# Kernel tuning notes

Measured on AMD Instinct MI355X. Metric: run time of the kernel, lower is better.

The kernel has to match this reference:

```python
import jax, jax.numpy as jnp
import numpy as np

NOISE_EPS = 0.01
TOP_K = 2


def setup_inputs() -> dict:
    key = jax.random.key(0)
    k1, k2, k3, k4 = jax.random.split(key, 4)
    B, S, D, E = 4, 4096, 2048, 64
    x = jax.random.normal(k1, (B, S, D), dtype=jnp.float32)
    raw_noise = jax.random.normal(k2, (B, S, E), dtype=jnp.float32)
    # gating_mlp: single Linear(D -> E), init std=0.02, zero bias
    W_gate = 0.02 * jax.random.normal(k3, (E, D), dtype=jnp.float32)
    b_gate = jnp.zeros((E,), dtype=jnp.float32)
    # noise_projection: Linear(D -> E, bias=False), init std=1/sqrt(D)
    W_noise = (1.0 / np.sqrt(D)) * jax.random.normal(k4, (E, D), dtype=jnp.float32)
    return {"x": x, "raw_noise": raw_noise, "W_gate": W_gate, "b_gate": b_gate, "W_noise": W_noise}


def reference(x, raw_noise, W_gate, b_gate, W_noise):
    # gate logits: [B,S,E]
    logits = jnp.einsum("bsd,ed->bse", x, W_gate) + b_gate
    # noisy top-k routing (training path)
    noise_stddev = jax.nn.softplus(jnp.einsum("bsd,ed->bse", x, W_noise)) + NOISE_EPS
    noisy = logits + raw_noise * noise_stddev
    top_v, top_i = jax.lax.top_k(noisy, TOP_K)            # [B,S,K]
    top_p = jax.nn.softmax(top_v.astype(jnp.float32), axis=-1).astype(noisy.dtype)
    B, S, E = noisy.shape
    T = B * S
    flat_logits = noisy.reshape(T, E)
    flat_i = top_i.reshape(T, TOP_K)
    flat_p = top_p.reshape(T, TOP_K)
    sparse = jnp.zeros((T, E), dtype=noisy.dtype).at[jnp.arange(T)[:, None], flat_i].set(flat_p)
    # aux load-balancing loss
    indicator = (sparse > 0.0).astype(jnp.float32)
    fraction_routed = indicator.sum(axis=0) / T           # f_e
    router_probs = jax.nn.softmax(flat_logits.astype(jnp.float32), axis=-1)
    avg_prob = router_probs.mean(axis=0)                  # p_e
    aux_loss = jnp.sum(fraction_routed * avg_prob) * E
    return sparse.reshape(B, S, E), aux_loss.astype(noisy.dtype)
```

## Files before the change

### kernel.cpp

```cpp
#include <hip/hip_runtime.h>
#include <math.h>

#define TOK 16384
#define DD  2048
#define EE  64
#define MT  32
#define KCW 32

typedef _Float16 half8  __attribute__((ext_vector_type(8)));
typedef float    floatx4 __attribute__((ext_vector_type(4)));

__global__ void build_wf(const float* __restrict__ Wg, const float* __restrict__ Wn,
                         _Float16* __restrict__ wf) {
  int tid  = blockIdx.x * 256 + threadIdx.x;
  int lane = tid & 63;
  int kc   = (tid >> 6) & 63;
  int ct   = tid >> 12;
  int col  = (ct & 3) * 16 + (lane & 15);
  int k    = kc * 32 + (lane >> 4) * 8;
  const float* W = (ct < 4) ? Wg : Wn;
  const float* src = W + (size_t)col * DD + k;
  float4 a = *reinterpret_cast<const float4*>(src);
  float4 b = *reinterpret_cast<const float4*>(src + 4);
  float v[8] = {a.x, a.y, a.z, a.w, b.x, b.y, b.z, b.w};
  half8 hi, lo;
#pragma unroll
  for (int j = 0; j < 8; ++j) {
    _Float16 h = (_Float16)v[j];
    hi[j] = h;
    lo[j] = (_Float16)(v[j] - (float)h);
  }
  size_t base = (((size_t)(kc * 8 + ct) * 2 + 0) * 64 + lane) * 8;
  *reinterpret_cast<half8*>(wf + base)       = hi;
  *reinterpret_cast<half8*>(wf + base + 512) = lo;
}

#define KBODY(kc, CUR, NXT)                                                        \
  {                                                                                \
    half8 Ah[2], Al[2];                                                            \
    _Pragma("unroll")                                                              \
    for (int mt = 0; mt < 2; ++mt) {                                               \
      float v[8] = {Aa[CUR][mt].x, Aa[CUR][mt].y, Aa[CUR][mt].z, Aa[CUR][mt].w,    \
                    Ab[CUR][mt].x, Ab[CUR][mt].y, Ab[CUR][mt].z, Ab[CUR][mt].w};   \
      _Pragma("unroll")                                                            \
      for (int j = 0; j < 8; ++j) {                                                \
        _Float16 h = (_Float16)v[j];                                               \
        Ah[mt][j] = h;                                                             \
        Al[mt][j] = (_Float16)(v[j] - (float)h);                                   \
      }                                                                            \
    }                                                                              \
    if ((kc) + 2 < KCW) {                                                          \
      _Pragma("unroll")                                                            \
      for (int mt = 0; mt < 2; ++mt) {                                             \
        Aa[CUR][mt] = *reinterpret_cast<const float4*>(xp[mt] + ((kc) + 2) * 32);  \
        Ab[CUR][mt] = *reinterpret_cast<const float4*>(xp[mt] + ((kc) + 2) * 32 + 4); \
      }                                                                            \
    }                                                                              \
    if ((kc) + 1 < KCW) {                                                          \
      _Pragma("unroll")                                                            \
      for (int f = 0; f < 16; ++f) Bf[NXT][f] = wp[((kc) + 1) * 1024 + f * 64];    \
    }                                                                              \
    _Pragma("unroll")                                                              \
    for (int mt = 0; mt < 2; ++mt)                                                 \
      _Pragma("unroll")                                                            \
      for (int ct = 0; ct < 8; ++ct)                                               \
        acc[mt][ct] = __builtin_amdgcn_mfma_f32_16x16x32_f16(                      \
            Ah[mt], Bf[CUR][ct * 2 + 0], acc[mt][ct], 0, 0, 0);                    \
    _Pragma("unroll")                                                              \
    for (int mt = 0; mt < 2; ++mt)                                                 \
      _Pragma("unroll")                                                            \
      for (int ct = 0; ct < 8; ++ct)                                               \
        acc[mt][ct] = __builtin_amdgcn_mfma_f32_16x16x32_f16(                      \
            Ah[mt], Bf[CUR][ct * 2 + 1], acc[mt][ct], 0, 0, 0);                    \
    _Pragma("unroll")                                                              \
    for (int mt = 0; mt < 2; ++mt)                                                 \
      _Pragma("unroll")                                                            \
      for (int ct = 0; ct < 8; ++ct)                                               \
        acc[mt][ct] = __builtin_amdgcn_mfma_f32_16x16x32_f16(                      \
            Al[mt], Bf[CUR][ct * 2 + 0], acc[mt][ct], 0, 0, 0);                    \
  }

__global__ __launch_bounds__(128, 1)
void gating_kernel(const float* __restrict__ x, const float* __restrict__ rn,
                   const _Float16* __restrict__ wf, const float* __restrict__ bg,
                   float* __restrict__ out,
                   float* __restrict__ cnt_g, float* __restrict__ psum_g) {
  __shared__ float Pacc[64 * 64];
  __shared__ float Vb[MT * 65];
  __shared__ float Eb[MT * 65];
  __shared__ float isum[MT];
  __shared__ int   ti[MT * 2];
  __shared__ float tp[MT * 2];

  const int t  = threadIdx.x;
  const int w  = t >> 6;
  const int l  = t & 63;
  const int q  = l >> 4;
  const int cl = l & 15;
  const int t0 = blockIdx.x * MT;

  const float* xp[2];
  xp[0] = x + (size_t)(t0 + cl) * DD + w * (KCW * 32) + q * 8;
  xp[1] = xp[0] + (size_t)16 * DD;

  const half8* wp = reinterpret_cast<const half8*>(wf) + (size_t)(w * KCW) * 16 * 64 + l;

  floatx4 acc[2][8];
#pragma unroll
  for (int mt = 0; mt < 2; ++mt)
#pragma unroll
    for (int ct = 0; ct < 8; ++ct) acc[mt][ct] = (floatx4)0.f;

  float4 Aa[2][2], Ab[2][2];
  half8  Bf[2][16];

#pragma unroll
  for (int mt = 0; mt < 2; ++mt) {
    Aa[0][mt] = *reinterpret_cast<const float4*>(xp[mt]);
    Ab[0][mt] = *reinterpret_cast<const float4*>(xp[mt] + 4);
    Aa[1][mt] = *reinterpret_cast<const float4*>(xp[mt] + 32);
    Ab[1][mt] = *reinterpret_cast<const float4*>(xp[mt] + 36);
  }
#pragma unroll
  for (int f = 0; f < 16; ++f) Bf[0][f] = wp[f * 64];

  for (int kc2 = 0; kc2 < KCW; kc2 += 2) {
    KBODY(kc2, 0, 1)
    KBODY(kc2 + 1, 1, 0)
  }

  if (w == 1) {
#pragma unroll
    for (int mt = 0; mt < 2; ++mt)
#pragma unroll
      for (int ct = 0; ct < 8; ++ct)
#pragma unroll
        for (int r = 0; r < 4; ++r)
          Pacc[((mt * 8 + ct) * 4 + r) * 64 + l] = acc[mt][ct][r];
  }
  __syncthreads();

  if (w == 0) {
#pragma unroll
    for (int mt = 0; mt < 2; ++mt)
#pragma unroll
      for (int ct = 0; ct < 8; ++ct)
#pragma unroll
        for (int r = 0; r < 4; ++r)
          acc[mt][ct][r] += Pacc[((mt * 8 + ct) * 4 + r) * 64 + l];

    float bgv[4];
#pragma unroll
    for (int ct = 0; ct < 4; ++ct) bgv[ct] = bg[ct * 16 + cl];

#pragma unroll
    for (int mt = 0; mt < 2; ++mt)
#pragma unroll
      for (int ct = 0; ct < 4; ++ct)
#pragma unroll
        for (int r = 0; r < 4; ++r) {
          const int tk = mt * 16 + q * 4 + r;
          const int c  = ct * 16 + cl;
          float gt = acc[mt][ct][r] + bgv[ct];
          float h  = acc[mt][ct + 4][r];
          float sp = (h > 20.f) ? h : log1pf(expf(h));
          float v  = gt + rn[(size_t)(t0 + tk) * EE + c] * (sp + 0.01f);
          Vb[tk * 65 + c] = v;
          Eb[tk * 65 + c] = expf(v);
        }
  }
  __syncthreads();

  if (t < MT) {
    float v1 = -1e30f, v2 = -1e30f;
    int   i1 = 0, i2 = 0;
    float s = 0.f;
    for (int e = 0; e < EE; ++e) {
      float v = Vb[t * 65 + e];
      s += Eb[t * 65 + e];
      if (v > v1)      { v2 = v1; i2 = i1; v1 = v; i1 = e; }
      else if (v > v2) { v2 = v;  i2 = e; }
    }
    isum[t] = 1.f / s;
    ti[t * 2 + 0] = i1; ti[t * 2 + 1] = i2;
    float e2 = expf(v2 - v1);
    float dn = 1.f + e2;
    tp[t * 2 + 0] = 1.f / dn;
    tp[t * 2 + 1] = e2 / dn;
  }
  __syncthreads();

#pragma unroll
  for (int i = 0; i < 4; ++i) {
    const int idx = t + i * 128;
    const int m   = idx >> 4;
    const int c0  = (idx & 15) * 4;
    const int i1 = ti[m * 2 + 0], i2 = ti[m * 2 + 1];
    const float p1 = tp[m * 2 + 0], p2 = tp[m * 2 + 1];
    float o[4];
#pragma unroll
    for (int j = 0; j < 4; ++j) {
      const int col = c0 + j;
      o[j] = (col == i1) ? p1 : ((col == i2) ? p2 : 0.f);
    }
    *reinterpret_cast<float4*>(out + (size_t)(t0 + m) * EE + c0) =
        make_float4(o[0], o[1], o[2], o[3]);
  }

  if (t < EE) {
    float s = 0.f;
    int   cn = 0;
#pragma unroll
    for (int m = 0; m < MT; ++m) {
      s  += Eb[m * 65 + t] * isum[m];
      cn += (ti[m * 2 + 0] == t) + (ti[m * 2 + 1] == t);
    }
    atomicAdd(&psum_g[t], s);
    atomicAdd(&cnt_g[t], (float)cn);
  }
}

__global__ void aux_kernel(const float* __restrict__ cnt_g,
                           const float* __restrict__ psum_g,
                           float* __restrict__ out) {
  int e = threadIdx.x;
  float v = cnt_g[e] * psum_g[e];
#pragma unroll
  for (int o = 32; o > 0; o >>= 1) v += __shfl_down(v, o);
  if (e == 0)
    out[(size_t)TOK * EE] = v * ((float)EE / ((float)TOK * (float)TOK));
}

extern "C" void kernel_launch(void* const* d_in, const int* in_sizes, int n_in,
                              void* d_out, int out_size, void* d_ws, size_t ws_size,
                              hipStream_t stream) {
  const float* x  = (const float*)d_in[0];
  const float* rn = (const float*)d_in[1];
  const float* Wg = (const float*)d_in[2];
  const float* bg = (const float*)d_in[3];
  const float* Wn = (const float*)d_in[4];
  float* out    = (float*)d_out;
  float* cnt_g  = (float*)d_ws;
  float* psum_g = cnt_g + EE;
  _Float16* wf  = (_Float16*)((float*)d_ws + 128);

  hipMemsetAsync(d_ws, 0, 2 * EE * sizeof(float), stream);
  build_wf<<<128, 256, 0, stream>>>(Wg, Wn, wf);
  gating_kernel<<<TOK / MT, 128, 0, stream>>>(x, rn, wf, bg, out, cnt_g, psum_g);
  aux_kernel<<<1, 64, 0, stream>>>(cnt_g, psum_g, out);
}
```

Baseline: 259.8 us.

## Split gating GEMM across 8 waves by column group and K half

```diff
diff --git a/kernel.cpp b/kernel.cpp
--- a/kernel.cpp
+++ b/kernel.cpp
@@ -30,144 +30,160 @@
     hi[j] = h;
     lo[j] = (_Float16)(v[j] - (float)h);
   }
-  size_t base = (((size_t)(kc * 8 + ct) * 2 + 0) * 64 + lane) * 8;
+  int cw4 = ct & 3;
+  int nf  = ct >> 2;
+  size_t base = (((size_t)(kc * 16 + cw4 * 4 + nf * 2) ) * 64 + lane) * 8;
   *reinterpret_cast<half8*>(wf + base)       = hi;
   *reinterpret_cast<half8*>(wf + base + 512) = lo;
 }
 
-#define KBODY(kc, CUR, NXT)                                                        \
-  {                                                                                \
-    half8 Ah[2], Al[2];                                                            \
-    _Pragma("unroll")                                                              \
-    for (int mt = 0; mt < 2; ++mt) {                                               \
-      float v[8] = {Aa[CUR][mt].x, Aa[CUR][mt].y, Aa[CUR][mt].z, Aa[CUR][mt].w,    \
-                    Ab[CUR][mt].x, Ab[CUR][mt].y, Ab[CUR][mt].z, Ab[CUR][mt].w};   \
-      _Pragma("unroll")                                                            \
-      for (int j = 0; j < 8; ++j) {                                                \
-        _Float16 h = (_Float16)v[j];                                               \
-        Ah[mt][j] = h;                                                             \
-        Al[mt][j] = (_Float16)(v[j] - (float)h);                                   \
-      }                                                                            \
-    }                                                                              \
-    if ((kc) + 2 < KCW) {                                                          \
-      _Pragma("unroll")                                                            \
-      for (int mt = 0; mt < 2; ++mt) {                                             \
-        Aa[CUR][mt] = *reinterpret_cast<const float4*>(xp[mt] + ((kc) + 2) * 32);  \
-        Ab[CUR][mt] = *reinterpret_cast<const float4*>(xp[mt] + ((kc) + 2) * 32 + 4); \
-      }                                                                            \
-    }                                                                              \
-    if ((kc) + 1 < KCW) {                                                          \
-      _Pragma("unroll")                                                            \
-      for (int f = 0; f < 16; ++f) Bf[NXT][f] = wp[((kc) + 1) * 1024 + f * 64];    \
-    }                                                                              \
-    _Pragma("unroll")                                                              \
-    for (int mt = 0; mt < 2; ++mt)                                                 \
-      _Pragma("unroll")                                                            \
-      for (int ct = 0; ct < 8; ++ct)                                               \
-        acc[mt][ct] = __builtin_amdgcn_mfma_f32_16x16x32_f16(                      \
-            Ah[mt], Bf[CUR][ct * 2 + 0], acc[mt][ct], 0, 0, 0);                    \
-    _Pragma("unroll")                                                              \
-    for (int mt = 0; mt < 2; ++mt)                                                 \
-      _Pragma("unroll")                                                            \
-      for (int ct = 0; ct < 8; ++ct)                                               \
-        acc[mt][ct] = __builtin_amdgcn_mfma_f32_16x16x32_f16(                      \
-            Ah[mt], Bf[CUR][ct * 2 + 1], acc[mt][ct], 0, 0, 0);                    \
-    _Pragma("unroll")                                                              \
-    for (int mt = 0; mt < 2; ++mt)                                                 \
-      _Pragma("unroll")                                                            \
-      for (int ct = 0; ct < 8; ++ct)                                               \
-        acc[mt][ct] = __builtin_amdgcn_mfma_f32_16x16x32_f16(                      \
-            Al[mt], Bf[CUR][ct * 2 + 0], acc[mt][ct], 0, 0, 0);                    \
-  }
-
-__global__ __launch_bounds__(128, 1)
+#define KBODY(CUR, NXT, AOFFE, BOFFH8, DOA, DOB)                                   \
+  {                                                                               \
+    half8 Ah[2], Al[2];                                                           \
+    _Pragma("unroll")                                                             \
+    for (int mt = 0; mt < 2; ++mt) {                                              \
+      float v[8] = {Aa[CUR][mt].x, Aa[CUR][mt].y, Aa[CUR][mt].z, Aa[CUR][mt].w,   \
+                    Ab[CUR][mt].x, Ab[CUR][mt].y, Ab[CUR][mt].z, Ab[CUR][mt].w};  \
+      _Pragma("unroll")                                                           \
+      for (int j = 0; j < 8; ++j) {                                               \
+        _Float16 h = (_Float16)v[j];                                              \
+        Ah[mt][j] = h;                                                            \
+        Al[mt][j] = (_Float16)(v[j] - (float)h);                                  \
+      }                                                                           \
+    }                                                                             \
+    if (DOA) {                                                                    \
+      Aa[CUR][0] = *reinterpret_cast<const float4*>(xq0 + (AOFFE));               \
+      Ab[CUR][0] = *reinterpret_cast<const float4*>(xq0 + (AOFFE) + 4);           \
+      Aa[CUR][1] = *reinterpret_cast<const float4*>(xq1 + (AOFFE));               \
+      Ab[CUR][1] = *reinterpret_cast<const float4*>(xq1 + (AOFFE) + 4);           \
+    }                                                                             \
+    if (DOB) {                                                                    \
+      _Pragma("unroll")                                                           \
+      for (int f = 0; f < 4; ++f) Bf[NXT][f] = wq[(BOFFH8) + f * 64];             \
+    }                                                                             \
+    _Pragma("unroll")                                                             \
+    for (int mt = 0; mt < 2; ++mt)                                                \
+      _Pragma("unroll")                                                           \
+      for (int nf = 0; nf < 2; ++nf)                                              \
+        acc[mt][nf] = __builtin_amdgcn_mfma_f32_16x16x32_f16(                     \
+            Ah[mt], Bf[CUR][nf * 2 + 0], acc[mt][nf], 0, 0, 0);                   \
+    _Pragma("unroll")                                                             \
+    for (int mt = 0; mt < 2; ++mt)                                                \
+      _Pragma("unroll")                                                           \
+      for (int nf = 0; nf < 2; ++nf)                                              \
+        acc[mt][nf] = __builtin_amdgcn_mfma_f32_16x16x32_f16(                     \
+            Ah[mt], Bf[CUR][nf * 2 + 1], acc[mt][nf], 0, 0, 0);                   \
+    _Pragma("unroll")                                                             \
+    for (int mt = 0; mt < 2; ++mt)                                                \
+      _Pragma("unroll")                                                           \
+      for (int nf = 0; nf < 2; ++nf)                                              \
+        acc[mt][nf] = __builtin_amdgcn_mfma_f32_16x16x32_f16(                     \
+            Al[mt], Bf[CUR][nf * 2 + 0], acc[mt][nf], 0, 0, 0);                   \
+  }
+
+__global__ __launch_bounds__(512, 4)
 void gating_kernel(const float* __restrict__ x, const float* __restrict__ rn,
                    const _Float16* __restrict__ wf, const float* __restrict__ bg,
                    float* __restrict__ out,
                    float* __restrict__ cnt_g, float* __restrict__ psum_g) {
-  __shared__ float Pacc[64 * 64];
+  __shared__ float Pacc[4096];
   __shared__ float Vb[MT * 65];
   __shared__ float Eb[MT * 65];
   __shared__ float isum[MT];
   __shared__ int   ti[MT * 2];
   __shared__ float tp[MT * 2];
 
-  const int t  = threadIdx.x;
-  const int w  = t >> 6;
-  const int l  = t & 63;
-  const int q  = l >> 4;
-  const int cl = l & 15;
-  const int t0 = blockIdx.x * MT;
-
-  const float* xp[2];
-  xp[0] = x + (size_t)(t0 + cl) * DD + w * (KCW * 32) + q * 8;
-  xp[1] = xp[0] + (size_t)16 * DD;
-
-  const half8* wp = reinterpret_cast<const half8*>(wf) + (size_t)(w * KCW) * 16 * 64 + l;
-
-  floatx4 acc[2][8];
+  const int t   = threadIdx.x;
+  const int w   = t >> 6;
+  const int cw4 = w & 3;
+  const int kw  = w >> 2;
+  const int l   = t & 63;
+  const int q   = l >> 4;
+  const int cl  = l & 15;
+  const int t0  = blockIdx.x * MT;
+
+  const float* xb0 = x + (size_t)(t0 + cl) * DD + kw * (KCW * 32) + q * 8;
+  const float* xb1 = xb0 + (size_t)16 * DD;
+
+  const half8* wb = reinterpret_cast<const half8*>(wf)
+                  + (size_t)kw * (KCW * 1024) + cw4 * 256 + l;
+
+  floatx4 acc[2][2];
 #pragma unroll
   for (int mt = 0; mt < 2; ++mt)
 #pragma unroll
-    for (int ct = 0; ct < 8; ++ct) acc[mt][ct] = (floatx4)0.f;
+    for (int nf = 0; nf < 2; ++nf) acc[mt][nf] = (floatx4)0.f;
 
   float4 Aa[2][2], Ab[2][2];
-  half8  Bf[2][16];
+  half8  Bf[2][4];
 
 #pragma unroll
   for (int mt = 0; mt < 2; ++mt) {
-    Aa[0][mt] = *reinterpret_cast<const float4*>(xp[mt]);
-    Ab[0][mt] = *reinterpret_cast<const float4*>(xp[mt] + 4);
-    Aa[1][mt] = *reinterpret_cast<const float4*>(xp[mt] + 32);
-    Ab[1][mt] = *reinterpret_cast<const float4*>(xp[mt] + 36);
-  }
-#pragma unroll
-  for (int f = 0; f < 16; ++f) Bf[0][f] = wp[f * 64];
-
-  for (int kc2 = 0; kc2 < KCW; kc2 += 2) {
-    KBODY(kc2, 0, 1)
-    KBODY(kc2 + 1, 1, 0)
-  }
-
-  if (w == 1) {
-#pragma unroll
-    for (int mt = 0; mt < 2; ++mt)
-#pragma unroll
-      for (int ct = 0; ct < 8; ++ct)
+    const float* xb = (mt == 0) ? xb0 : xb1;
+    Aa[0][mt] = *reinterpret_cast<const float4*>(xb);
+    Ab[0][mt] = *reinterpret_cast<const float4*>(xb + 4);
+    Aa[1][mt] = *reinterpret_cast<const float4*>(xb + 32);
+    Ab[1][mt] = *reinterpret_cast<const float4*>(xb + 36);
+  }
+#pragma unroll
+  for (int f = 0; f < 4; ++f) Bf[0][f] = wb[f * 64];
+
+  const float* xq0 = xb0 + 64;
+  const float* xq1 = xb1 + 64;
+  const half8* wq  = wb + 1024;
+
+  for (int it = 0; it < (KCW - 2) / 2; ++it) {
+    KBODY(0, 1, 0, 0, 1, 1)
+    KBODY(1, 0, 32, 1024, 1, 1)
+    xq0 += 64; xq1 += 64; wq += 2048;
+  }
+  KBODY(0, 1, 0, 0, 0, 1)
+  KBODY(1, 0, 0, 0, 0, 0)
+
+  float bgv = 0.f;
+  float rnv[2][4];
+  if (kw == 0) {
+    bgv = bg[cw4 * 16 + cl];
+#pragma unroll
+    for (int mt = 0; mt < 2; ++mt)
+#pragma unroll
+      for (int r = 0; r < 4; ++r)
+        rnv[mt][r] = rn[(size_t)(t0 + mt * 16 + q * 4 + r) * EE + cw4 * 16 + cl];
+  }
+
+  if (kw == 1) {
+#pragma unroll
+    for (int mt = 0; mt < 2; ++mt)
+#pragma unroll
+      for (int nf = 0; nf < 2; ++nf)
 #pragma unroll
         for (int r = 0; r < 4; ++r)
-          Pacc[((mt * 8 + ct) * 4 + r) * 64 + l] = acc[mt][ct][r];
+          Pacc[(cw4 * 16 + (mt * 2 + nf) * 4 + r) * 64 + l] = acc[mt][nf][r];
   }
   __syncthreads();
 
-  if (w == 0) {
-#pragma unroll
-    for (int mt = 0; mt < 2; ++mt)
-#pragma unroll
-      for (int ct = 0; ct < 8; ++ct)
+  if (kw == 0) {
+#pragma unroll
+    for (int mt = 0; mt < 2; ++mt)
+#pragma unroll
+      for (int nf = 0; nf < 2; ++nf)
 #pragma unroll
         for (int r = 0; r < 4; ++r)
-          acc[mt][ct][r] += Pacc[((mt * 8 + ct) * 4 + r) * 64 + l];
-
-    float bgv[4];
-#pragma unroll
-    for (int ct = 0; ct < 4; ++ct) bgv[ct] = bg[ct * 16 + cl];
-
-#pragma unroll
-    for (int mt = 0; mt < 2; ++mt)
-#pragma unroll
-      for (int ct = 0; ct < 4; ++ct)
-#pragma unroll
-        for (int r = 0; r < 4; ++r) {
-          const int tk = mt * 16 + q * 4 + r;
-          const int c  = ct * 16 + cl;
-          float gt = acc[mt][ct][r] + bgv[ct];
-          float h  = acc[mt][ct + 4][r];
-          float sp = (h > 20.f) ? h : log1pf(expf(h));
-          float v  = gt + rn[(size_t)(t0 + tk) * EE + c] * (sp + 0.01f);
-          Vb[tk * 65 + c] = v;
-          Eb[tk * 65 + c] = expf(v);
-        }
+          acc[mt][nf][r] += Pacc[(cw4 * 16 + (mt * 2 + nf) * 4 + r) * 64 + l];
+
+#pragma unroll
+    for (int mt = 0; mt < 2; ++mt)
+#pragma unroll
+      for (int r = 0; r < 4; ++r) {
+        const int tk = mt * 16 + q * 4 + r;
+        const int c  = cw4 * 16 + cl;
+        float gt = acc[mt][0][r] + bgv;
+        float h  = acc[mt][1][r];
+        float sp = (h > 20.f) ? h : log1pf(expf(h));
+        float v  = gt + rnv[mt][r] * (sp + 0.01f);
+        Vb[tk * 65 + c] = v;
+        Eb[tk * 65 + c] = expf(v);
+      }
   }
   __syncthreads();
 
@@ -190,11 +206,9 @@
   }
   __syncthreads();
 
-#pragma unroll
-  for (int i = 0; i < 4; ++i) {
-    const int idx = t + i * 128;
-    const int m   = idx >> 4;
-    const int c0  = (idx & 15) * 4;
+  {
+    const int m  = t >> 4;
+    const int c0 = (t & 15) * 4;
     const int i1 = ti[m * 2 + 0], i2 = ti[m * 2 + 1];
     const float p1 = tp[m * 2 + 0], p2 = tp[m * 2 + 1];
     float o[4];
@@ -246,6 +260,6 @@
 
   hipMemsetAsync(d_ws, 0, 2 * EE * sizeof(float), stream);
   build_wf<<<128, 256, 0, stream>>>(Wg, Wn, wf);
-  gating_kernel<<<TOK / MT, 128, 0, stream>>>(x, rn, wf, bg, out, cnt_g, psum_g);
+  gating_kernel<<<TOK / MT, 512, 0, stream>>>(x, rn, wf, bg, out, cnt_g, psum_g);
   aux_kernel<<<1, 64, 0, stream>>>(cnt_g, psum_g, out);
 }
```

Measured after the change: 263.5 us. Within noise of the previous version (+1.4%).
